# Optimization experiments

Hardware: AMD Instinct MI355X
Metric: run time of the kernel (lower is better)

The kernel has to match this reference:

```python
import jax, jax.numpy as jnp
import numpy as np

C = 8           # feat_channel
B, N = 8, 64    # batch, max objects
H, W = 128, 128
D = (C + 2) * C + C + C * C + C + C + 1  # 169


def setup_inputs() -> dict:
    key = jax.random.key(0)
    k1, k2, k3, k4 = jax.random.split(key, 4)
    seg_feat = jax.random.normal(k1, (B, C, H, W), dtype=jnp.float32)
    conv_weight = jax.random.normal(k2, (B, D, H, W), dtype=jnp.float32)
    mask = jnp.ones((B, N), dtype=jnp.float32)
    ind = jax.random.randint(k3, (B, N), 0, H * W, dtype=jnp.int64)
    target = jax.random.uniform(k4, (B, N, H, W), dtype=jnp.float32)
    return {"seg_feat": seg_feat, "conv_weight": conv_weight, "mask": mask,
            "ind": ind, "target": target}


def reference(seg_feat, conv_weight, mask, ind, target):
    b, c, h, w = seg_feat.shape
    n = ind.shape[1]
    # _tranpose_and_gather_feat: [B,D,H,W] -> [B,HW,D] -> gather at ind -> [B,N,D]
    wflat = conv_weight.reshape(b, -1, h * w).transpose(0, 2, 1)
    weight = jnp.take_along_axis(wflat, ind[:, :, None], axis=1)  # [B,N,D]
    splits = np.cumsum([(c + 2) * c, c, c * c, c, c])
    w1, b1, w2, b2, w3, b3 = jnp.split(weight, splits, axis=-1)
    w1 = w1.reshape(b, n, c, c + 2)   # per-object conv1 1x1 weights
    w2 = w2.reshape(b, n, c, c)
    w3 = w3.reshape(b, n, 1, c)
    # object centers and relative coordinate maps
    x0 = (ind % w).astype(jnp.float32)
    y0 = (ind // w).astype(jnp.float32)
    xg = jnp.arange(w, dtype=jnp.float32)
    yg = jnp.arange(h, dtype=jnp.float32)
    y_grid, x_grid = jnp.meshgrid(yg, xg, indexing="ij")  # [H,W]
    x_rel = (x_grid[None, None] - x0[:, :, None, None]) / 128.0  # [B,N,H,W]
    y_rel = (y_grid[None, None] - y0[:, :, None, None]) / 128.0
    feat = jnp.concatenate(
        [jnp.broadcast_to(seg_feat[:, None], (b, n, c, h, w)),
         x_rel[:, :, None], y_rel[:, :, None]], axis=2)  # [B,N,C+2,H,W]
    # three grouped 1x1 convs == per-object channel contractions
    h1 = jax.nn.relu(jnp.einsum("bnoc,bnchw->bnohw", w1, feat) + b1[..., None, None])
    h2 = jax.nn.relu(jnp.einsum("bnoc,bnchw->bnohw", w2, h1) + b2[..., None, None])
    out = jax.nn.sigmoid(jnp.einsum("bnoc,bnchw->bnohw", w3, h2) + b3[..., None, None])[:, :, 0]  # [B,N,H,W]
    m = mask[:, :, None, None]
    pred = out * m
    tgt = target * m
    smooth = 1.0
    inter = jnp.sum(pred * tgt, axis=(1, 2, 3))
    denom = jnp.sum(pred * pred, axis=(1, 2, 3)) + jnp.sum(tgt * tgt, axis=(1, 2, 3))
    loss = 1.0 - (2.0 * inter + smooth) / (denom + smooth)  # per-image dice
    return jnp.mean(loss)  # sum over batch / batch_size
```

## Files before the change

kernel.cpp:

```cpp
#include <hip/hip_runtime.h>

#define Cc 8
#define Hh 128
#define Ww 128
#define Nn 64
#define Bb 8
#define Dd 169
#define HW (Hh * Ww)
#define NP 4
#define NPG 8
#define PXS 1024
#define NSTRIPE (HW / PXS)
#define NBLK (Bb * NPG * NSTRIPE)
#define FRAGW 16
#define FRAG_U32 (256 * 64 * FRAGW)
#define SLOTS (NPG * NSTRIPE)

#define INV128 (1.0f / 128.0f)

typedef __fp16 f16x2 __attribute__((ext_vector_type(2)));
typedef _Float16 h8 __attribute__((ext_vector_type(8)));
typedef float f32x4 __attribute__((ext_vector_type(4)));

static __device__ __forceinline__ uint32_t pku(float a, float b) {
    f16x2 t = __builtin_amdgcn_cvt_pkrtz(a, b);
    uint32_t u; __builtin_memcpy(&u, &t, 4); return u;
}
static __device__ __forceinline__ h8 u4h8(uint32_t a, uint32_t b, uint32_t c, uint32_t d) {
    uint32_t u[4] = {a, b, c, d}; h8 r; __builtin_memcpy(&r, u, 16); return r;
}

__global__ void pack_frags(const float* __restrict__ conv_weight,
                           const float* __restrict__ mask,
                           const int*   __restrict__ ind,
                           uint32_t*    __restrict__ frag) {
    const int npair = blockIdx.x;
    const int b     = npair >> 5;
    const int bn0   = b * Nn + 2 * (npair & 31);
    const int l  = threadIdx.x;
    const int g  = l >> 4, r = l & 15, rr = r & 7;
    const int bnr = bn0 + (r >> 3);
    const int bng = bn0 + (g >> 1);
    const float* base = conv_weight + (size_t)b * Dd * HW;
    const float* srcR = base + ind[bnr];
    const float* srcG = base + ind[bng];

    float a1[8];
    #pragma unroll
    for (int e = 0; e < 8; ++e) {
        const int k = 8 * g + e;
        float v = 0.f;
        if (k < 8)       v = srcR[(size_t)(rr * 10 + k) * HW];
        else if (k == 8) v = srcR[(size_t)(rr * 10 + 8) * HW];
        else if (k == 9) v = srcR[(size_t)(rr * 10 + 9) * HW];
        else if (k == 10) {
            const float w8 = srcR[(size_t)(rr * 10 + 8) * HW];
            const float w9 = srcR[(size_t)(rr * 10 + 9) * HW];
            const float b1 = srcR[(size_t)(80 + rr) * HW];
            const int   ib = ind[bnr];
            v = b1 - w8 * ((float)(ib & 127) * INV128)
                   - w9 * ((float)(ib >> 7) * INV128);
        }
        a1[e] = v;
    }
    float a2[4];
    #pragma unroll
    for (int e = 0; e < 4; ++e) {
        const int k2 = 4 * g + e;
        float v = 0.f;
        if (r < 8)  { if (k2 < 8)  v = srcR[(size_t)(88 + rr * 8 + k2) * HW]; }
        else        { if (k2 >= 8) v = srcR[(size_t)(88 + rr * 8 + (k2 - 8)) * HW]; }
        a2[e] = v;
    }
    float w3v[4], c2v[4];
    #pragma unroll
    for (int j = 0; j < 4; ++j) {
        const int c = (4 * g + j) & 7;
        w3v[j] = srcG[(size_t)(160 + c) * HW];
        c2v[j] = srcG[(size_t)(152 + c) * HW];
    }
    const float b3 = srcG[(size_t)168 * HW];
    const float mm = mask[bng];
    const float fl = (g == 0 || g == 2) ? mm * mm : 0.f;

    uint32_t* dst = frag + ((size_t)npair * 64 + l) * FRAGW;
    dst[0] = pku(a1[0], a1[1]); dst[1] = pku(a1[2], a1[3]);
    dst[2] = pku(a1[4], a1[5]); dst[3] = pku(a1[6], a1[7]);
    dst[4] = pku(a2[0], a2[1]); dst[5] = pku(a2[2], a2[3]);
    float* df = (float*)dst;
    df[6] = w3v[0]; df[7] = w3v[1]; df[8] = w3v[2]; df[9] = w3v[3];
    df[10] = c2v[0]; df[11] = c2v[1]; df[12] = c2v[2]; df[13] = c2v[3];
    df[14] = b3; df[15] = fl;
}

__global__ __launch_bounds__(256)
void seg_dice_main(const float* __restrict__ seg_feat,
                   const float* __restrict__ target,
                   const uint32_t* __restrict__ frag,
                   float* __restrict__ red_base) {
    const int bid    = blockIdx.x;
    const int b      = bid & 7;
    const int rest   = bid >> 3;
    const int npg    = rest & 7;
    const int stripe = rest >> 3;
    const int p0     = stripe * PXS;
    const int tid  = threadIdx.x;
    const int wave = tid >> 6;
    const int l    = tid & 63;
    const int g    = l >> 4, col = l & 15;

    __shared__ uint4 lds4[PXS];

    const float* seg_b = seg_feat + (size_t)b * Cc * HW;
    #pragma unroll
    for (int q = 0; q < 4; ++q) {
        const int px = q * 256 + tid;
        float v[8];
        #pragma unroll
        for (int c = 0; c < 8; ++c) v[c] = seg_b[(size_t)c * HW + p0 + px];
        lds4[px] = uint4{pku(v[0], v[1]), pku(v[2], v[3]),
                         pku(v[4], v[5]), pku(v[6], v[7])};
    }

    const int npair0 = b * 32 + npg * NP;
    uint32_t A1u[NP][4], A2u[NP][2];
    float w3v[NP][4], c2v[NP][4], b3v[NP], flv[NP];
    int bnl[NP];
    #pragma unroll
    for (int j = 0; j < NP; ++j) {
        const uint4* fp = (const uint4*)(frag + ((size_t)(npair0 + j) * 64 + l) * FRAGW);
        const uint4 q0 = fp[0], q1 = fp[1], q2 = fp[2], q3 = fp[3];
        A1u[j][0] = q0.x; A1u[j][1] = q0.y; A1u[j][2] = q0.z; A1u[j][3] = q0.w;
        A2u[j][0] = q1.x; A2u[j][1] = q1.y;
        w3v[j][0] = __uint_as_float(q1.z); w3v[j][1] = __uint_as_float(q1.w);
        w3v[j][2] = __uint_as_float(q2.x); w3v[j][3] = __uint_as_float(q2.y);
        c2v[j][0] = __uint_as_float(q2.z); c2v[j][1] = __uint_as_float(q2.w);
        c2v[j][2] = __uint_as_float(q3.x); c2v[j][3] = __uint_as_float(q3.y);
        b3v[j] = __uint_as_float(q3.z);
        flv[j] = __uint_as_float(q3.w);
        bnl[j] = b * Nn + 2 * (npg * NP + j) + (l >> 5);
    }
    __syncthreads();

    const f32x4 ZF = {0.f, 0.f, 0.f, 0.f};
    float inter = 0.f, ps = 0.f, ts = 0.f;

    #pragma unroll 1
    for (int tt = wave; tt < PXS / 16; tt += 4) {
        const int pxt = tt * 16;
        const int pxg = p0 + pxt + col;

        const uint4 d = lds4[pxt + col];
        const uint32_t xv = pku((float)(pxg & 127) * INV128,
                                (float)(pxg >> 7) * INV128);
        const uint32_t ov = pku(1.f, 0.f);
        const uint32_t e0 = (g == 0) ? d.x : ((g == 1) ? xv : 0u);
        const uint32_t e1 = (g == 0) ? d.y : ((g == 1) ? ov : 0u);
        const uint32_t e2 = (g == 0) ? d.z : 0u;
        const uint32_t e3 = (g == 0) ? d.w : 0u;
        const h8 B1 = u4h8(e0, e1, e2, e3);

        #pragma unroll
        for (int j = 0; j < NP; ++j) {
            const h8 A1 = u4h8(A1u[j][0], A1u[j][1], A1u[j][2], A1u[j][3]);
            f32x4 h1 = __builtin_amdgcn_mfma_f32_16x16x32_f16(A1, B1, ZF, 0, 0, 0);
            h1[0] = fmaxf(h1[0], 0.f); h1[1] = fmaxf(h1[1], 0.f);
            h1[2] = fmaxf(h1[2], 0.f); h1[3] = fmaxf(h1[3], 0.f);

            const h8 B2 = u4h8(pku(h1[0], h1[1]), pku(h1[2], h1[3]), 0u, 0u);
            const h8 A2 = u4h8(A2u[j][0], A2u[j][1], 0u, 0u);
            f32x4 c2; c2[0] = c2v[j][0]; c2[1] = c2v[j][1];
                      c2[2] = c2v[j][2]; c2[3] = c2v[j][3];
            f32x4 h2 = __builtin_amdgcn_mfma_f32_16x16x32_f16(A2, B2, c2, 0, 0, 0);
            h2[0] = fmaxf(h2[0], 0.f); h2[1] = fmaxf(h2[1], 0.f);
            h2[2] = fmaxf(h2[2], 0.f); h2[3] = fmaxf(h2[3], 0.f);

            float zp = h2[0] * w3v[j][0];
            zp = fmaf(h2[1], w3v[j][1], zp);
            zp = fmaf(h2[2], w3v[j][2], zp);
            zp = fmaf(h2[3], w3v[j][3], zp);
            zp += __shfl_xor(zp, 16);
            const float z  = zp + b3v[j];
            const float o  = __builtin_amdgcn_rcpf(1.f + __expf(-z));
            const float tv = target[(size_t)bnl[j] * HW + pxg];
            const float fo = flv[j] * o;
            inter = fmaf(fo, tv, inter);
            ps    = fmaf(fo, o, ps);
            ts    = fmaf(flv[j], tv * tv, ts);
        }
    }

    #pragma unroll
    for (int off = 32; off > 0; off >>= 1) {
        inter += __shfl_down(inter, off);
        ps    += __shfl_down(ps,    off);
        ts    += __shfl_down(ts,    off);
    }
    __shared__ float red[3][4];
    if ((tid & 63) == 0) { red[0][wave] = inter; red[1][wave] = ps; red[2][wave] = ts; }
    __syncthreads();
    if (tid == 0) {
        red_base[(b * 3 + 0) * SLOTS + rest] = red[0][0] + red[0][1] + red[0][2] + red[0][3];
        red_base[(b * 3 + 1) * SLOTS + rest] = red[1][0] + red[1][1] + red[1][2] + red[1][3];
        red_base[(b * 3 + 2) * SLOTS + rest] = red[2][0] + red[2][1] + red[2][2] + red[2][3];
    }
}

__global__ void seg_dice_final(const float* __restrict__ red_base, float* __restrict__ out) {
    __shared__ float red[24][4];
    const int tid = threadIdx.x;
    if (tid < 96) {
        const int series = tid >> 2;
        const int part   = tid & 3;
        const float4* p = (const float4*)(red_base + series * SLOTS + part * 32);
        float s = 0.f;
        #pragma unroll
        for (int i = 0; i < 8; ++i) { const float4 v = p[i]; s += (v.x + v.y) + (v.z + v.w); }
        red[series][part] = s;
    }
    __syncthreads();
    if (tid == 0) {
        float acc = 0.f;
        #pragma unroll
        for (int b = 0; b < Bb; ++b) {
            const float inter = red[b*3+0][0] + red[b*3+0][1] + red[b*3+0][2] + red[b*3+0][3];
            const float p2    = red[b*3+1][0] + red[b*3+1][1] + red[b*3+1][2] + red[b*3+1][3];
            const float t2    = red[b*3+2][0] + red[b*3+2][1] + red[b*3+2][2] + red[b*3+2][3];
            acc += 1.0f - (2.0f * inter + 1.0f) / (p2 + t2 + 1.0f);
        }
        out[0] = acc * (1.0f / (float)Bb);
    }
}

extern "C" void kernel_launch(void* const* d_in, const int* in_sizes, int n_in,
                              void* d_out, int out_size, void* d_ws, size_t ws_size,
                              hipStream_t stream) {
    const float* seg_feat    = (const float*)d_in[0];
    const float* conv_weight = (const float*)d_in[1];
    const float* mask        = (const float*)d_in[2];
    const int*   ind         = (const int*)d_in[3];
    const float* target      = (const float*)d_in[4];
    float* out = (float*)d_out;

    uint32_t* fragtab  = (uint32_t*)d_ws;
    float*    red_base = (float*)d_ws + FRAG_U32;

    pack_frags<<<256, 64, 0, stream>>>(conv_weight, mask, ind, fragtab);
    seg_dice_main<<<NBLK, 256, 0, stream>>>(seg_feat, target, fragtab, red_base);
    seg_dice_final<<<1, 128, 0, stream>>>(red_base, out);
}
```

Before: 38.64 us.

## Halve pixel stripe and split sigmoid/target work across lane groups by object parity

Pixel stripes shrink from 1024 to 512, doubling the block count for better occupancy and load balance, with the final reduction widened to match. In the inner loop, objects are processed in pairs. Lane groups g=0/2 and g=1/3 now each handle the epilogue (sigmoid, target load, accumulation) for a different object in the pair instead of half the lanes idling. This halves redundant exp/rcp and target loads per object. The cost is more blocks re-staging seg_feat and per-thread fragment loads, plus slightly more selection logic.

```diff
diff --git a/kernel.cpp b/kernel.cpp
--- a/kernel.cpp
+++ b/kernel.cpp
@@ -9,7 +9,7 @@
 #define HW (Hh * Ww)
 #define NP 4
 #define NPG 8
-#define PXS 1024
+#define PXS 512
 #define NSTRIPE (HW / PXS)
 #define NBLK (Bb * NPG * NSTRIPE)
 #define FRAGW 16
@@ -81,7 +81,7 @@
     }
     const float b3 = srcG[(size_t)168 * HW];
     const float mm = mask[bng];
-    const float fl = (g == 0 || g == 2) ? mm * mm : 0.f;
+    const float fl = mm * mm;
 
     uint32_t* dst = frag + ((size_t)npair * 64 + l) * FRAGW;
     dst[0] = pku(a1[0], a1[1]); dst[1] = pku(a1[2], a1[3]);
@@ -113,7 +113,7 @@
 
     const float* seg_b = seg_feat + (size_t)b * Cc * HW;
     #pragma unroll
-    for (int q = 0; q < 4; ++q) {
+    for (int q = 0; q < 2; ++q) {
         const int px = q * 256 + tid;
         float v[8];
         #pragma unroll
@@ -125,7 +125,6 @@
     const int npair0 = b * 32 + npg * NP;
     uint32_t A1u[NP][4], A2u[NP][2];
     float w3v[NP][4], c2v[NP][4], b3v[NP], flv[NP];
-    int bnl[NP];
     #pragma unroll
     for (int j = 0; j < NP; ++j) {
         const uint4* fp = (const uint4*)(frag + ((size_t)(npair0 + j) * 64 + l) * FRAGW);
@@ -138,7 +137,18 @@
         c2v[j][2] = __uint_as_float(q3.x); c2v[j][3] = __uint_as_float(q3.y);
         b3v[j] = __uint_as_float(q3.z);
         flv[j] = __uint_as_float(q3.w);
-        bnl[j] = b * Nn + 2 * (npg * NP + j) + (l >> 5);
+    }
+
+    const int par = g & 1;
+    float flS[2], b3S[2];
+    const float* ptrS[2];
+    #pragma unroll
+    for (int s = 0; s < 2; ++s) {
+        const int jj = 2 * s + par;
+        flS[s] = par ? flv[2 * s + 1] : flv[2 * s];
+        b3S[s] = par ? b3v[2 * s + 1] : b3v[2 * s];
+        const int bnS = b * Nn + 2 * (npg * NP + jj) + (l >> 5);
+        ptrS[s] = target + (size_t)bnS * HW + p0 + col;
     }
     __syncthreads();
 
@@ -161,32 +171,46 @@
         const h8 B1 = u4h8(e0, e1, e2, e3);
 
         #pragma unroll
-        for (int j = 0; j < NP; ++j) {
-            const h8 A1 = u4h8(A1u[j][0], A1u[j][1], A1u[j][2], A1u[j][3]);
-            f32x4 h1 = __builtin_amdgcn_mfma_f32_16x16x32_f16(A1, B1, ZF, 0, 0, 0);
-            h1[0] = fmaxf(h1[0], 0.f); h1[1] = fmaxf(h1[1], 0.f);
-            h1[2] = fmaxf(h1[2], 0.f); h1[3] = fmaxf(h1[3], 0.f);
-
-            const h8 B2 = u4h8(pku(h1[0], h1[1]), pku(h1[2], h1[3]), 0u, 0u);
-            const h8 A2 = u4h8(A2u[j][0], A2u[j][1], 0u, 0u);
-            f32x4 c2; c2[0] = c2v[j][0]; c2[1] = c2v[j][1];
-                      c2[2] = c2v[j][2]; c2[3] = c2v[j][3];
-            f32x4 h2 = __builtin_amdgcn_mfma_f32_16x16x32_f16(A2, B2, c2, 0, 0, 0);
-            h2[0] = fmaxf(h2[0], 0.f); h2[1] = fmaxf(h2[1], 0.f);
-            h2[2] = fmaxf(h2[2], 0.f); h2[3] = fmaxf(h2[3], 0.f);
-
-            float zp = h2[0] * w3v[j][0];
-            zp = fmaf(h2[1], w3v[j][1], zp);
-            zp = fmaf(h2[2], w3v[j][2], zp);
-            zp = fmaf(h2[3], w3v[j][3], zp);
-            zp += __shfl_xor(zp, 16);
-            const float z  = zp + b3v[j];
+        for (int s = 0; s < 2; ++s) {
+            const int jA = 2 * s, jB = 2 * s + 1;
+            const h8 A1a = u4h8(A1u[jA][0], A1u[jA][1], A1u[jA][2], A1u[jA][3]);
+            const h8 A1b = u4h8(A1u[jB][0], A1u[jB][1], A1u[jB][2], A1u[jB][3]);
+            f32x4 h1a = __builtin_amdgcn_mfma_f32_16x16x32_f16(A1a, B1, ZF, 0, 0, 0);
+            f32x4 h1b = __builtin_amdgcn_mfma_f32_16x16x32_f16(A1b, B1, ZF, 0, 0, 0);
+            #pragma unroll
+            for (int e = 0; e < 4; ++e) {
+                h1a[e] = fmaxf(h1a[e], 0.f);
+                h1b[e] = fmaxf(h1b[e], 0.f);
+            }
+            const h8 B2a = u4h8(pku(h1a[0], h1a[1]), pku(h1a[2], h1a[3]), 0u, 0u);
+            const h8 B2b = u4h8(pku(h1b[0], h1b[1]), pku(h1b[2], h1b[3]), 0u, 0u);
+            const h8 A2a = u4h8(A2u[jA][0], A2u[jA][1], 0u, 0u);
+            const h8 A2b = u4h8(A2u[jB][0], A2u[jB][1], 0u, 0u);
+            f32x4 c2a; c2a[0] = c2v[jA][0]; c2a[1] = c2v[jA][1];
+                       c2a[2] = c2v[jA][2]; c2a[3] = c2v[jA][3];
+            f32x4 c2b; c2b[0] = c2v[jB][0]; c2b[1] = c2v[jB][1];
+                       c2b[2] = c2v[jB][2]; c2b[3] = c2v[jB][3];
+            f32x4 h2a = __builtin_amdgcn_mfma_f32_16x16x32_f16(A2a, B2a, c2a, 0, 0, 0);
+            f32x4 h2b = __builtin_amdgcn_mfma_f32_16x16x32_f16(A2b, B2b, c2b, 0, 0, 0);
+
+            float zpa = fmaxf(h2a[0], 0.f) * w3v[jA][0];
+            zpa = fmaf(fmaxf(h2a[1], 0.f), w3v[jA][1], zpa);
+            zpa = fmaf(fmaxf(h2a[2], 0.f), w3v[jA][2], zpa);
+            zpa = fmaf(fmaxf(h2a[3], 0.f), w3v[jA][3], zpa);
+            float zpb = fmaxf(h2b[0], 0.f) * w3v[jB][0];
+            zpb = fmaf(fmaxf(h2b[1], 0.f), w3v[jB][1], zpb);
+            zpb = fmaf(fmaxf(h2b[2], 0.f), w3v[jB][2], zpb);
+            zpb = fmaf(fmaxf(h2b[3], 0.f), w3v[jB][3], zpb);
+            zpa += __shfl_xor(zpa, 16);
+            zpb += __shfl_xor(zpb, 16);
+
+            const float z  = (par ? zpb : zpa) + b3S[s];
             const float o  = __builtin_amdgcn_rcpf(1.f + __expf(-z));
-            const float tv = target[(size_t)bnl[j] * HW + pxg];
-            const float fo = flv[j] * o;
+            const float tv = ptrS[s][pxt];
+            const float fo = flS[s] * o;
             inter = fmaf(fo, tv, inter);
             ps    = fmaf(fo, o, ps);
-            ts    = fmaf(flv[j], tv * tv, ts);
+            ts    = fmaf(flS[s], tv * tv, ts);
         }
     }
 
@@ -212,10 +236,10 @@
     if (tid < 96) {
         const int series = tid >> 2;
         const int part   = tid & 3;
-        const float4* p = (const float4*)(red_base + series * SLOTS + part * 32);
+        const float4* p = (const float4*)(red_base + series * SLOTS + part * 64);
         float s = 0.f;
         #pragma unroll
-        for (int i = 0; i < 8; ++i) { const float4 v = p[i]; s += (v.x + v.y) + (v.z + v.w); }
+        for (int i = 0; i < 16; ++i) { const float4 v = p[i]; s += (v.x + v.y) + (v.z + v.w); }
         red[series][part] = s;
     }
     __syncthreads();
```

Result: slower. 59.82 us (+54.8%).
